# Optimization experiments

Hardware: AMD Instinct MI355X
Metric: run time of the kernel (lower is better)

## Reference

```python
import jax, jax.numpy as jnp
import numpy as np

N, K, C, L = 8192, 12, 128, 6
FF = 4 * C
SIG_LO, SIG_HI = 1.0, 5.0
BOX = 25.0

TRI_NAMES = ("ln_g", "ln_b", "Wa", "ba", "Wga", "bga", "Wb", "bb", "Wgb", "bgb",
             "lno_g", "lno_b", "Wo", "bo", "Wgo", "bgo")
FFN_NAMES = ("ln_g", "ln_b", "W1", "b1", "W2", "b2")


def _ln(x, g, b, eps=1e-5):
    m = jnp.mean(x, axis=-1, keepdims=True)
    v = jnp.mean((x - m) ** 2, axis=-1, keepdims=True)
    return (x - m) * jax.lax.rsqrt(v + eps) * g + b


def _knn_embed(coords):
    # pairwise distances -> k smallest (self included), Gaussian RBF bank over C sigmas
    d2 = jnp.sum((coords[:, None, :] - coords[None, :, :]) ** 2, axis=-1)  # [N,N]
    dist = jnp.sqrt(jnp.maximum(d2, 0.0))
    neg_d, nbr = jax.lax.top_k(-dist, K)                      # [N,K]
    k_dist = -neg_d
    sig = jnp.linspace(SIG_LO, SIG_HI, C)                     # [C]
    g = jnp.exp(-(k_dist[..., None] ** 2) / (2.0 * sig ** 2))  # [N,K,C]
    vals = jnp.where(g > 0.1, g, 0.0)                         # threshold as in repo
    vals = jnp.where(jnp.isnan(vals), 0.0, vals)
    return nbr, vals


def _transpose_vals(v, nbr):
    # sparse rowcol_transpose: value of edge (j,i) aligned to slot of edge (i,j); 0 if absent
    n = nbr.shape[0]
    nn = nbr[nbr]                                   # [N,K,K]: neighbor lists of each neighbor j
    eq = nn == jnp.arange(n)[:, None, None]         # slot where j lists i back
    pos = jnp.argmax(eq, axis=-1)                   # [N,K]
    found = jnp.any(eq, axis=-1)                    # [N,K]
    tv = v[nbr, pos]                                # [N,K,C] value at edge (j,i)
    return jnp.where(found[..., None], tv, jnp.zeros_like(tv))


def _tri_update(v, nbr, p, incoming):
    x = _ln(v, p["ln_g"], p["ln_b"])
    a = jax.nn.sigmoid(x @ p["Wga"] + p["bga"]) * (x @ p["Wa"] + p["ba"])
    b = jax.nn.sigmoid(x @ p["Wgb"] + p["bgb"]) * (x @ p["Wb"] + p["bb"])
    if incoming:  # column/incoming update operates on transposed edges
        a = _transpose_vals(a, nbr)
        b = _transpose_vals(b, nbr)
    # sparse triangle multiplicative update over KNN neighbor slots
    k = jnp.einsum('ntc,nmtc->nmc', a, b[nbr])      # [N,K,C]
    o = _ln(k, p["lno_g"], p["lno_b"]) @ p["Wo"] + p["bo"]
    return jax.nn.sigmoid(x @ p["Wgo"] + p["bgo"]) * o


def _ffn(v, p):
    x = _ln(v, p["ln_g"], p["ln_b"])
    return jax.nn.gelu(x @ p["W1"] + p["b1"], approximate=False) @ p["W2"] + p["b2"]


def _forward(coords, tri, ffn, dec_W, dec_b):
    nbr, v = _knn_embed(coords)
    v = jax.lax.stop_gradient(v)  # embedding runs under torch.no_grad in the original

    def step(v, lp):
        tp, fp = lp
        p_row = {n: t[0] for n, t in zip(TRI_NAMES, tp)}
        p_col = {n: t[1] for n, t in zip(TRI_NAMES, tp)}
        v = v + _tri_update(v, nbr, p_row, False)   # row (outgoing) update
        v = v + _tri_update(v, nbr, p_col, True)    # col (incoming) update
        v = v + _ffn(v, dict(zip(FFN_NAMES, fp)))
        return v, None

    v, _ = jax.lax.scan(jax.checkpoint(step), v, (tri, ffn))
    s = v + _transpose_vals(v, nbr)                 # sparse_operation(edge, edge^T, op='sum')
    e = s @ dec_W + dec_b                           # [N,K,1] decode
    rows = jnp.repeat(jnp.arange(N), K)
    dense = jnp.zeros((N, N, e.shape[-1]), e.dtype)
    dense = dense.at[rows, nbr.reshape(-1)].add(e.reshape(-1, e.shape[-1]))
    return dense                                    # [N,N,1] like .to_dense()


def setup_inputs() -> dict:
    key = jax.random.key(0)
    ks = jax.random.split(key, 8)
    coords = jax.random.uniform(ks[0], (N, 3), jnp.float32) * BOX

    def lin(k, fin, fout, pre=()):
        kw, _ = jax.random.split(k)
        W = jax.random.normal(kw, pre + (fin, fout), jnp.float32) / np.sqrt(fin).astype(np.float32)
        b = jnp.zeros(pre + (fout,), jnp.float32)
        return W, b

    inp = {"coords": coords}
    k_iter = iter(jax.random.split(ks[1], 16))
    pre = (L, 2)
    inp["tri_ln_g"] = jnp.ones(pre + (C,), jnp.float32)
    inp["tri_ln_b"] = jnp.zeros(pre + (C,), jnp.float32)
    for nm in ("a", "ga", "b", "gb", "o", "go"):
        W, b = lin(next(k_iter), C, C, pre)
        inp[f"tri_W{nm}"] = W
        inp[f"tri_b{nm}"] = b
    inp["tri_lno_g"] = jnp.ones(pre + (C,), jnp.float32)
    inp["tri_lno_b"] = jnp.zeros(pre + (C,), jnp.float32)
    inp["ffn_ln_g"] = jnp.ones((L, C), jnp.float32)
    inp["ffn_ln_b"] = jnp.zeros((L, C), jnp.float32)
    inp["ffn_W1"], inp["ffn_b1"] = lin(next(k_iter), C, FF, (L,))
    inp["ffn_W2"], inp["ffn_b2"] = lin(next(k_iter), FF, C, (L,))
    inp["dec_W"], inp["dec_b"] = lin(next(k_iter), C, 1)
    return inp


def reference(coords, tri_ln_g, tri_ln_b, tri_Wa, tri_ba, tri_Wga, tri_bga,
              tri_Wb, tri_bb, tri_Wgb, tri_bgb, tri_lno_g, tri_lno_b,
              tri_Wo, tri_bo, tri_Wgo, tri_bgo,
              ffn_ln_g, ffn_ln_b, ffn_W1, ffn_b1, ffn_W2, ffn_b2,
              dec_W, dec_b):
    tri = (tri_ln_g, tri_ln_b, tri_Wa, tri_ba, tri_Wga, tri_bga,
           tri_Wb, tri_bb, tri_Wgb, tri_bgb, tri_lno_g, tri_lno_b,
           tri_Wo, tri_bo, tri_Wgo, tri_bgo)
    ffn = (ffn_ln_g, ffn_ln_b, ffn_W1, ffn_b1, ffn_W2, ffn_b2)
    return _forward(coords, tri, ffn, dec_W, dec_b)
```

## Files before the change

kernel.cpp:

```cpp
#include <hip/hip_runtime.h>
#include <hip/hip_bf16.h>
#include <stdint.h>
#include <stddef.h>

#define NPTS 8192
#define KNN  12
#define CH   128
#define FFD  512
#define MEDGE (NPTS * KNN)
#define NCELL 512

typedef __attribute__((ext_vector_type(8))) _Float16 half8;
typedef __attribute__((ext_vector_type(4))) _Float16 half4;
typedef __attribute__((ext_vector_type(4))) float f32x4;

__device__ __forceinline__ float wave_sum(float v) {
#pragma unroll
  for (int off = 32; off > 0; off >>= 1) v += __shfl_xor(v, off, 64);
  return v;
}
__device__ __forceinline__ float sigm_(float x) { return 1.0f / (1.0f + expf(-x)); }
__device__ __forceinline__ float gelu_(float x) { return 0.5f * x * (1.0f + erff(x * 0.7071067811865475f)); }

#define HADDR(row, ch) ((((row) * 64 + ((ch) ^ ((row) & 7)))) * 8)

__device__ __forceinline__ int morton3(int x, int y, int z) {
  int m = 0;
#pragma unroll
  for (int b = 0; b < 3; ++b)
    m |= (((x >> b) & 1) << (3 * b + 2)) | (((y >> b) & 1) << (3 * b + 1)) | (((z >> b) & 1) << (3 * b));
  return m;
}

__global__ __launch_bounds__(512)
void zero_hist(int* __restrict__ hist)
{
  hist[threadIdx.x] = 0;
}

__global__ __launch_bounds__(256)
void prep_coords(const float* __restrict__ c, float4* __restrict__ c4,
                 int* __restrict__ cell, int* __restrict__ hist)
{
  int i = blockIdx.x * 256 + threadIdx.x;
  if (i >= NPTS) return;
  float x = c[3 * i], y = c[3 * i + 1], z = c[3 * i + 2];
  c4[i] = make_float4(x, y, z, 0.0f);
  int cx = (int)(x * (8.0f / 25.0f)); if (cx > 7) cx = 7; if (cx < 0) cx = 0;
  int cy = (int)(y * (8.0f / 25.0f)); if (cy > 7) cy = 7; if (cy < 0) cy = 0;
  int cz = (int)(z * (8.0f / 25.0f)); if (cz > 7) cz = 7; if (cz < 0) cz = 0;
  int cl = morton3(cx, cy, cz);
  cell[i] = cl;
  atomicAdd(&hist[cl], 1);
}

__global__ __launch_bounds__(512)
void prefix512(const int* __restrict__ hist, int* __restrict__ base)
{
  __shared__ int tmp[NCELL];
  int t = threadIdx.x;
  tmp[t] = hist[t];
  __syncthreads();
  for (int off = 1; off < NCELL; off <<= 1) {
    int v = tmp[t];
    if (t >= off) v += tmp[t - off];
    __syncthreads();
    tmp[t] = v;
    __syncthreads();
  }
  base[t] = tmp[t] - hist[t];
}

__global__ __launch_bounds__(256)
void scatter_perm(const int* __restrict__ cell, int* __restrict__ base,
                  int* __restrict__ rank, int* __restrict__ perm)
{
  int i = blockIdx.x * 256 + threadIdx.x;
  if (i >= NPTS) return;
  int r = atomicAdd(&base[cell[i]], 1);
  rank[i] = r;
  perm[r] = i;
}

struct SwzArgs {
  const float* src[8];
  _Float16* dst[8];
  int K[8], N[8], B[8], perB[8];
};

__global__ __launch_bounds__(256)
void prep_weights_swz(SwzArgs sa)
{
  int g = blockIdx.y;
  int idx = blockIdx.x * 256 + threadIdx.x;
  int perB = sa.perB[g];
  if (idx >= sa.B[g] * perB) return;
  int K = sa.K[g], N = sa.N[g];
  int b = idx / perB;
  int c = idx - b * perB;
  int l16 = c & 15;
  int quad = (c >> 4) & 3;
  int rest = c >> 6;
  int kts = K >> 5;
  int kt = rest % kts;
  int mt = rest / kts;
  const float* sp = sa.src[g] + ((size_t)b * K + kt * 32 + quad * 8) * N + mt * 16 + l16;
  _Float16* dp = sa.dst[g] + ((size_t)b * perB + c) * 8;
#pragma unroll
  for (int e = 0; e < 8; ++e) dp[e] = (_Float16)sp[(size_t)e * N];
}

#define KNN_CAP 2048

__global__ __launch_bounds__(256)
void knn_embed(const float4* __restrict__ coords4, const int* __restrict__ perm,
               const int* __restrict__ rank,
               const float* __restrict__ lng, const float* __restrict__ lnb,
               int* __restrict__ nbr, float* __restrict__ v0, _Float16* __restrict__ xln)
{
#pragma clang fp contract(off)
  __shared__ unsigned long long buf[KNN_CAP];
  __shared__ unsigned long long sel[KNN];
  __shared__ int cnt_s;
  const int i = blockIdx.x;
  const int tid = threadIdx.x;
  const int lane = tid & 63;
  const int wv = tid >> 6;
  const float4 ci = coords4[perm[i]];

  float T2 = 9.0f;
  int cnt;
  while (true) {
    if (tid == 0) cnt_s = 0;
    __syncthreads();
    for (int j = tid; j < NPTS; j += 256) {
      float4 cj = coords4[j];
      float dx = ci.x - cj.x;
      float dy = ci.y - cj.y;
      float dz = ci.z - cj.z;
      float d2 = dx * dx + dy * dy + dz * dz;
      if (d2 < T2) {
        unsigned long long key =
            (((unsigned long long)__float_as_uint(sqrtf(d2))) << 32) | (unsigned int)j;
        int idx = atomicAdd(&cnt_s, 1);
        if (idx < KNN_CAP) buf[idx] = key;
      }
    }
    __syncthreads();
    cnt = cnt_s;
    if (cnt >= KNN) break;
    T2 *= 4.0f;
    __syncthreads();
  }
  if (cnt > KNN_CAP) cnt = KNN_CAP;

  if (wv == 0) {
    unsigned long long best[KNN];
#pragma unroll
    for (int q = 0; q < KNN; ++q) best[q] = ~0ULL;
    for (int p2 = lane; p2 < cnt; p2 += 64) {
      unsigned long long key = buf[p2];
      if (key < best[KNN - 1]) {
        best[KNN - 1] = key;
#pragma unroll
        for (int q = KNN - 2; q >= 0; --q) {
          if (best[q + 1] < best[q]) { unsigned long long t = best[q]; best[q] = best[q + 1]; best[q + 1] = t; }
        }
      }
    }
    int p = 0;
    for (int r = 0; r < KNN; ++r) {
      unsigned long long c = ~0ULL;
#pragma unroll
      for (int q = 0; q < KNN; ++q) if (q == p) c = best[q];
      unsigned long long m = c;
#pragma unroll
      for (int off = 32; off > 0; off >>= 1) {
        unsigned long long o = __shfl_xor(m, off, 64);
        if (o < m) m = o;
      }
      if (c == m) ++p;
      if (lane == 0) sel[r] = m;
    }
  }
  __syncthreads();
  if (tid < KNN)
    nbr[i * KNN + tid] = rank[(int)(unsigned int)(sel[tid] & 0xFFFFFFFFULL)];

  float g1 = lng[lane], g2 = lng[lane + 64];
  float bb1 = lnb[lane], bb2 = lnb[lane + 64];
  for (int k = wv * 3; k < wv * 3 + 3; ++k) {
    float d = __uint_as_float((unsigned int)(sel[k] >> 32));
    float sig1 = (float)(1.0 + 4.0 * (double)lane / 127.0);
    float sig2 = (float)(1.0 + 4.0 * (double)(lane + 64) / 127.0);
    float e1 = expf((-(d * d)) / (2.0f * sig1 * sig1));
    float e2 = expf((-(d * d)) / (2.0f * sig2 * sig2));
    float v1 = (e1 > 0.1f) ? e1 : 0.0f;
    float v2 = (e2 > 0.1f) ? e2 : 0.0f;
    size_t off = (size_t)(i * KNN + k) * CH;
    v0[off + lane] = v1;
    v0[off + lane + 64] = v2;
    float m = wave_sum(v1 + v2) * (1.0f / 128.0f);
    float d1 = v1 - m, d2 = v2 - m;
    float var = wave_sum(d1 * d1 + d2 * d2) * (1.0f / 128.0f);
    float rs = 1.0f / sqrtf(var + 1e-5f);
    xln[off + lane]      = (_Float16)(d1 * rs * g1 + bb1);
    xln[off + lane + 64] = (_Float16)(d2 * rs * g2 + bb2);
  }
}

__global__ __launch_bounds__(256)
void build_tidx(const int* __restrict__ nbr, int* __restrict__ tidx)
{
  int e = blockIdx.x * 256 + threadIdx.x;
  if (e >= MEDGE) return;
  int i = e / KNN;
  int j = nbr[e];
  int res = -1;
#pragma unroll
  for (int t = 0; t < KNN; ++t) {
    if (nbr[j * KNN + t] == i) { res = j * KNN + t; break; }
  }
  tidx[e] = res;
}

__global__ __launch_bounds__(256)
void gemm_ab_go(const _Float16* __restrict__ xln,
                const _Float16* __restrict__ wa,  const float* __restrict__ ba,
                const _Float16* __restrict__ wga, const float* __restrict__ bga,
                const _Float16* __restrict__ wb,  const float* __restrict__ bb,
                const _Float16* __restrict__ wgb, const float* __restrict__ bgb,
                const _Float16* __restrict__ wgo, const float* __restrict__ bgo,
                _Float16* __restrict__ aout, _Float16* __restrict__ bout,
                _Float16* __restrict__ gobout)
{
  const int lane = threadIdx.x & 63;
  const int quad = lane >> 4;
  const int l16 = lane & 15;
  const int gw = blockIdx.x * 4 + (threadIdx.x >> 6);
  const int base = gw * 32;
  const int chbase = quad * 16 + l16;

  half8 xf[2][4];
#pragma unroll
  for (int rt = 0; rt < 2; ++rt)
#pragma unroll
    for (int kt = 0; kt < 4; ++kt)
      xf[rt][kt] = *(const half8*)(xln + (size_t)(base + rt * 16 + l16) * CH + kt * 32 + quad * 8);

  const half8* WA  = (const half8*)wa;
  const half8* WGA = (const half8*)wga;
  const half8* WB  = (const half8*)wb;
  const half8* WGB = (const half8*)wgb;
  const half8* WGO = (const half8*)wgo;

#pragma unroll
  for (int mt = 0; mt < 8; ++mt) {
    f32x4 aA[2], aGA[2], aB[2], aGB[2], aGO[2];
    const f32x4 z = {0.f, 0.f, 0.f, 0.f};
#pragma unroll
    for (int rt = 0; rt < 2; ++rt) { aA[rt] = z; aGA[rt] = z; aB[rt] = z; aGB[rt] = z; aGO[rt] = z; }
#pragma unroll
    for (int kt = 0; kt < 4; ++kt) {
      int ch = (mt * 4 + kt) * 64 + chbase;
      half8 wfa = WA[ch], wfga = WGA[ch], wfb = WB[ch], wfgb = WGB[ch], wfgo = WGO[ch];
#pragma unroll
      for (int rt = 0; rt < 2; ++rt) {
        aA[rt]  = __builtin_amdgcn_mfma_f32_16x16x32_f16(wfa,  xf[rt][kt], aA[rt], 0, 0, 0);
        aGA[rt] = __builtin_amdgcn_mfma_f32_16x16x32_f16(wfga, xf[rt][kt], aGA[rt], 0, 0, 0);
        aB[rt]  = __builtin_amdgcn_mfma_f32_16x16x32_f16(wfb,  xf[rt][kt], aB[rt], 0, 0, 0);
        aGB[rt] = __builtin_amdgcn_mfma_f32_16x16x32_f16(wfgb, xf[rt][kt], aGB[rt], 0, 0, 0);
        aGO[rt] = __builtin_amdgcn_mfma_f32_16x16x32_f16(wfgo, xf[rt][kt], aGO[rt], 0, 0, 0);
      }
    }
    f32x4 bva  = *(const f32x4*)(ba  + mt * 16 + quad * 4);
    f32x4 bvga = *(const f32x4*)(bga + mt * 16 + quad * 4);
    f32x4 bvb  = *(const f32x4*)(bb  + mt * 16 + quad * 4);
    f32x4 bvgb = *(const f32x4*)(bgb + mt * 16 + quad * 4);
    f32x4 bvgo = *(const f32x4*)(bgo + mt * 16 + quad * 4);
#pragma unroll
    for (int rt = 0; rt < 2; ++rt) {
      half4 av, bv, gv;
#pragma unroll
      for (int r = 0; r < 4; ++r) {
        av[r] = (_Float16)(sigm_(aGA[rt][r] + bvga[r]) * (aA[rt][r] + bva[r]));
        bv[r] = (_Float16)(sigm_(aGB[rt][r] + bvgb[r]) * (aB[rt][r] + bvb[r]));
        gv[r] = (_Float16)(sigm_(aGO[rt][r] + bvgo[r]));
      }
      size_t off = (size_t)(base + rt * 16 + l16) * CH + mt * 16 + quad * 4;
      *(half4*)(aout + off) = av;
      *(half4*)(bout + off) = bv;
      *(half4*)(gobout + off) = gv;
    }
  }
}

__global__ __launch_bounds__(192)
void tri_og(const _Float16* __restrict__ a, const _Float16* __restrict__ b,
            const int* __restrict__ nbr, const int* __restrict__ tidx,
            const float* __restrict__ lng, const float* __restrict__ lnb,
            const _Float16* __restrict__ wo, const float* __restrict__ bo,
            const _Float16* __restrict__ gob, float* __restrict__ v,
            const float* __restrict__ nlng, const float* __restrict__ nlnb,
            _Float16* __restrict__ xlnN, int incoming)
{
  __shared__ alignas(16) _Float16 As[48][136];
  __shared__ alignas(16) _Float16 klds[48][136];
  __shared__ int bidx[4][KNN][KNN];
  __shared__ int nbr_s[4][KNN];
  const int blk = blockIdx.x;
  const int n0 = ((blk & 7) * 256 + (blk >> 3)) * 4;
  const int tid = threadIdx.x;

  if (tid < 48) nbr_s[tid / KNN][tid % KNN] = nbr[n0 * KNN + tid];
  __syncthreads();
  for (int it = tid; it < 4 * KNN * KNN; it += 192) {
    int nn = it / (KNN * KNN);
    int r = it - nn * KNN * KNN;
    int m = r / KNN, t = r - m * KNN;
    int j = nbr_s[nn][m];
    bidx[nn][m][t] = incoming ? tidx[j * KNN + t] : (j * KNN + t);
  }
  for (int it = tid; it < 4 * KNN * 16; it += 192) {
    int nn = it / (KNN * 16);
    int r = it - nn * (KNN * 16);
    int t = r >> 4;
    int c8 = (r & 15) * 8;
    half8 av;
    if (incoming) {
      int ti = tidx[(size_t)(n0 + nn) * KNN + t];
      if (ti >= 0) av = *(const half8*)(a + (size_t)ti * CH + c8);
      else {
#pragma unroll
        for (int e = 0; e < 8; ++e) av[e] = (_Float16)0.0f;
      }
    } else {
      av = *(const half8*)(a + (size_t)((n0 + nn) * KNN + t) * CH + c8);
    }
    *(half8*)&As[nn * KNN + t][c8] = av;
  }
  __syncthreads();

  const int m2 = tid >> 4;
  const int c8 = (tid & 15) * 8;
  for (int nn = 0; nn < 4; ++nn) {
    float acc[8];
#pragma unroll
    for (int r = 0; r < 8; ++r) acc[r] = 0.0f;
#pragma unroll
    for (int t = 0; t < KNN; ++t) {
      int bi = bidx[nn][m2][t];
      if (bi >= 0) {
        half8 bv = *(const half8*)(b + (size_t)bi * CH + c8);
        half8 av = *(const half8*)&As[nn * KNN + t][c8];
#pragma unroll
        for (int r = 0; r < 8; ++r) acc[r] += (float)av[r] * (float)bv[r];
      }
    }
    float s = 0.0f, sq = 0.0f;
#pragma unroll
    for (int r = 0; r < 8; ++r) { s += acc[r]; sq += acc[r] * acc[r]; }
#pragma unroll
    for (int off = 1; off < 16; off <<= 1) {
      s += __shfl_xor(s, off, 64);
      sq += __shfl_xor(sq, off, 64);
    }
    float mean = s * (1.0f / 128.0f);
    float var = sq * (1.0f / 128.0f) - mean * mean;
    if (var < 0.0f) var = 0.0f;
    float rs = 1.0f / sqrtf(var + 1e-5f);
    half8 o;
#pragma unroll
    for (int r = 0; r < 8; ++r)
      o[r] = (_Float16)((acc[r] - mean) * rs * lng[c8 + r] + lnb[c8 + r]);
    *(half8*)&klds[nn * KNN + m2][c8] = o;
  }
  __syncthreads();

  const int lane = tid & 63;
  const int w = tid >> 6;
  const int quad = lane >> 4;
  const int l16 = lane & 15;
  const int chbase = quad * 16 + l16;
  const size_t rowOff = (size_t)(n0 * KNN + w * 16 + l16) * CH;

  half8 kf[4];
#pragma unroll
  for (int kt = 0; kt < 4; ++kt)
    kf[kt] = *(const half8*)&klds[w * 16 + l16][kt * 32 + quad * 8];

  const half8* WO = (const half8*)wo;
  f32x4 vn[8];
  float s = 0.0f, sq = 0.0f;
#pragma unroll
  for (int mt = 0; mt < 8; ++mt) {
    f32x4 acc = {0.f, 0.f, 0.f, 0.f};
#pragma unroll
    for (int kt = 0; kt < 4; ++kt)
      acc = __builtin_amdgcn_mfma_f32_16x16x32_f16(WO[(mt * 4 + kt) * 64 + chbase], kf[kt], acc, 0, 0, 0);
    half4 g4 = *(const half4*)(gob + rowOff + mt * 16 + quad * 4);
    f32x4 bo4 = *(const f32x4*)(bo + mt * 16 + quad * 4);
    f32x4 vv = *(const f32x4*)(v + rowOff + mt * 16 + quad * 4);
#pragma unroll
    for (int r = 0; r < 4; ++r) {
      float nv = vv[r] + (float)g4[r] * (acc[r] + bo4[r]);
      vn[mt][r] = nv;
      s += nv;
      sq += nv * nv;
    }
    *(f32x4*)(v + rowOff + mt * 16 + quad * 4) = vn[mt];
  }
  s  += __shfl_xor(s, 16, 64);  s  += __shfl_xor(s, 32, 64);
  sq += __shfl_xor(sq, 16, 64); sq += __shfl_xor(sq, 32, 64);
  float mean = s * (1.0f / 128.0f);
  float var = sq * (1.0f / 128.0f) - mean * mean;
  if (var < 0.0f) var = 0.0f;
  float rs = 1.0f / sqrtf(var + 1e-5f);
#pragma unroll
  for (int mt = 0; mt < 8; ++mt) {
    f32x4 g4 = *(const f32x4*)(nlng + mt * 16 + quad * 4);
    f32x4 b4 = *(const f32x4*)(nlnb + mt * 16 + quad * 4);
    half4 o;
#pragma unroll
    for (int r = 0; r < 4; ++r)
      o[r] = (_Float16)((vn[mt][r] - mean) * rs * g4[r] + b4[r]);
    *(half4*)(xlnN + rowOff + mt * 16 + quad * 4) = o;
  }
}

__global__ __launch_bounds__(256)
void ffn_fused(const _Float16* __restrict__ xln,
               const _Float16* __restrict__ w1, const float* __restrict__ b1,
               const _Float16* __restrict__ w2, const float* __restrict__ b2,
               float* __restrict__ v,
               const float* __restrict__ nlng, const float* __restrict__ nlnb,
               _Float16* __restrict__ xlnN)
{
  __shared__ alignas(16) _Float16 hlds[32 * FFD];
  __shared__ float part[32][4][2];
  const int tid = threadIdx.x;
  const int lane = tid & 63;
  const int w = tid >> 6;
  const int quad = lane >> 4;
  const int l16 = lane & 15;
  const int rowBase = blockIdx.x * 32;
  const int chbase = quad * 16 + l16;

  half8 xf[2][4];
#pragma unroll
  for (int rt = 0; rt < 2; ++rt)
#pragma unroll
    for (int kt = 0; kt < 4; ++kt)
      xf[rt][kt] = *(const half8*)(xln + (size_t)(rowBase + rt * 16 + l16) * CH + kt * 32 + quad * 8);

  const half8* W1 = (const half8*)w1;
#pragma unroll
  for (int mt = 0; mt < 8; ++mt) {
    int mtg = w * 8 + mt;
    f32x4 acc[2];
    const f32x4 z = {0.f, 0.f, 0.f, 0.f};
    acc[0] = z; acc[1] = z;
#pragma unroll
    for (int kt = 0; kt < 4; ++kt) {
      half8 wf = W1[(mtg * 4 + kt) * 64 + chbase];
#pragma unroll
      for (int rt = 0; rt < 2; ++rt)
        acc[rt] = __builtin_amdgcn_mfma_f32_16x16x32_f16(wf, xf[rt][kt], acc[rt], 0, 0, 0);
    }
    f32x4 bv = *(const f32x4*)(b1 + mtg * 16 + quad * 4);
    int ch = mtg * 2 + (quad >> 1);
    int sub = (quad & 1) * 4;
#pragma unroll
    for (int rt = 0; rt < 2; ++rt) {
      int row = rt * 16 + l16;
      half4 hh;
#pragma unroll
      for (int r = 0; r < 4; ++r)
        hh[r] = (_Float16)(gelu_(acc[rt][r] + bv[r]));
      *(half4*)&hlds[HADDR(row, ch) + sub] = hh;
    }
  }
  __syncthreads();

  const half8* W2 = (const half8*)w2;
  f32x4 vn2[2][2];
  float s2[2] = {0.f, 0.f}, q2[2] = {0.f, 0.f};
#pragma unroll
  for (int m2 = 0; m2 < 2; ++m2) {
    int mt = w * 2 + m2;
    f32x4 accA[2], accB[2];
    const f32x4 z = {0.f, 0.f, 0.f, 0.f};
    accA[0] = z; accA[1] = z; accB[0] = z; accB[1] = z;
#pragma unroll
    for (int kt = 0; kt < 16; kt += 2) {
      half8 wf0 = W2[(mt * 16 + kt) * 64 + chbase];
      half8 wf1 = W2[(mt * 16 + kt + 1) * 64 + chbase];
#pragma unroll
      for (int rt = 0; rt < 2; ++rt) {
        int row = rt * 16 + l16;
        half8 hf0 = *(const half8*)&hlds[HADDR(row, kt * 4 + quad)];
        half8 hf1 = *(const half8*)&hlds[HADDR(row, (kt + 1) * 4 + quad)];
        accA[rt] = __builtin_amdgcn_mfma_f32_16x16x32_f16(wf0, hf0, accA[rt], 0, 0, 0);
        accB[rt] = __builtin_amdgcn_mfma_f32_16x16x32_f16(wf1, hf1, accB[rt], 0, 0, 0);
      }
    }
    f32x4 bv = *(const f32x4*)(b2 + mt * 16 + quad * 4);
#pragma unroll
    for (int rt = 0; rt < 2; ++rt) {
      size_t off = (size_t)(rowBase + rt * 16 + l16) * CH + mt * 16 + quad * 4;
      f32x4 vv = *(const f32x4*)(v + off);
#pragma unroll
      for (int r = 0; r < 4; ++r) {
        float nv = vv[r] + accA[rt][r] + accB[rt][r] + bv[r];
        vn2[m2][rt][r] = nv;
        s2[rt] += nv;
        q2[rt] += nv * nv;
      }
      *(f32x4*)(v + off) = vn2[m2][rt];
    }
  }
#pragma unroll
  for (int rt = 0; rt < 2; ++rt) {
    float ss = s2[rt], qq = q2[rt];
    ss += __shfl_xor(ss, 16, 64); ss += __shfl_xor(ss, 32, 64);
    qq += __shfl_xor(qq, 16, 64); qq += __shfl_xor(qq, 32, 64);
    if (quad == 0) { part[rt * 16 + l16][w][0] = ss; part[rt * 16 + l16][w][1] = qq; }
  }
  __syncthreads();
#pragma unroll
  for (int rt = 0; rt < 2; ++rt) {
    int row = rt * 16 + l16;
    float su = part[row][0][0] + part[row][1][0] + part[row][2][0] + part[row][3][0];
    float qu = part[row][0][1] + part[row][1][1] + part[row][2][1] + part[row][3][1];
    float mean = su * (1.0f / 128.0f);
    float var = qu * (1.0f / 128.0f) - mean * mean;
    if (var < 0.0f) var = 0.0f;
    float rs = 1.0f / sqrtf(var + 1e-5f);
#pragma unroll
    for (int m2 = 0; m2 < 2; ++m2) {
      int mt = w * 2 + m2;
      f32x4 g4 = *(const f32x4*)(nlng + mt * 16 + quad * 4);
      f32x4 b4 = *(const f32x4*)(nlnb + mt * 16 + quad * 4);
      half4 o;
#pragma unroll
      for (int r = 0; r < 4; ++r)
        o[r] = (_Float16)((vn2[m2][rt][r] - mean) * rs * g4[r] + b4[r]);
      *(half4*)(xlnN + (size_t)(rowBase + row) * CH + mt * 16 + quad * 4) = o;
    }
  }
}

__global__ __launch_bounds__(256)
void decode_row(const float* __restrict__ vin, const int* __restrict__ tidx,
                const int* __restrict__ nbr, const int* __restrict__ perm,
                const float* __restrict__ decW, const float* __restrict__ decB,
                float* __restrict__ out)
{
  __shared__ float ev[KNN];
  __shared__ int col_s[KNN];
  const int n = blockIdx.x;
  const int tid = threadIdx.x;
  const int lane = tid & 63;
  const int w = tid >> 6;
  if (tid < KNN) col_s[tid] = perm[nbr[n * KNN + tid]];
  float dw1 = decW[lane], dw2 = decW[lane + 64];
  for (int k = w; k < KNN; k += 4) {
    int e = n * KNN + k;
    int ti = tidx[e];
    float s1 = vin[(size_t)e * CH + lane];
    float s2 = vin[(size_t)e * CH + 64 + lane];
    if (ti >= 0) {
      s1 += vin[(size_t)ti * CH + lane];
      s2 += vin[(size_t)ti * CH + 64 + lane];
    }
    float tot = wave_sum(s1 * dw1 + s2 * dw2);
    if (lane == 0) ev[k] = tot + decB[0];
  }
  __syncthreads();
  const int orig_n = perm[n];
  float4 z = make_float4(0.f, 0.f, 0.f, 0.f);
  float4* row = (float4*)(out + (size_t)orig_n * NPTS);
  for (int idx = tid; idx < NPTS / 4; idx += 256) row[idx] = z;
  __syncthreads();
  if (tid < KNN) out[(size_t)orig_n * NPTS + col_s[tid]] = ev[tid];
}

extern "C" void kernel_launch(void* const* d_in, const int* in_sizes, int n_in,
                              void* d_out, int out_size, void* d_ws, size_t ws_size,
                              hipStream_t stream)
{
  (void)in_sizes; (void)n_in; (void)out_size; (void)ws_size;
  const float* coords  = (const float*)d_in[0];
  const float* t_ln_g  = (const float*)d_in[1];
  const float* t_ln_b  = (const float*)d_in[2];
  const float* t_Wa    = (const float*)d_in[3];
  const float* t_ba    = (const float*)d_in[4];
  const float* t_Wga   = (const float*)d_in[5];
  const float* t_bga   = (const float*)d_in[6];
  const float* t_Wb    = (const float*)d_in[7];
  const float* t_bb    = (const float*)d_in[8];
  const float* t_Wgb   = (const float*)d_in[9];
  const float* t_bgb   = (const float*)d_in[10];
  const float* t_Wo    = (const float*)d_in[11];
  const float* t_bo    = (const float*)d_in[12];
  const float* t_Wgo   = (const float*)d_in[13];
  const float* t_bgo   = (const float*)d_in[14];
  const float* t_lno_g = (const float*)d_in[15];
  const float* t_lno_b = (const float*)d_in[16];
  const float* f_ln_g  = (const float*)d_in[17];
  const float* f_ln_b  = (const float*)d_in[18];
  const float* f_W1    = (const float*)d_in[19];
  const float* f_b1    = (const float*)d_in[20];
  const float* f_W2    = (const float*)d_in[21];
  const float* f_b2    = (const float*)d_in[22];
  const float* dec_W   = (const float*)d_in[23];
  const float* dec_b   = (const float*)d_in[24];

  const size_t NKC = (size_t)MEDGE * CH;
  char* ws = (char*)d_ws;
  float* v        = (float*)(ws);
  _Float16* gx    = (_Float16*)(ws + NKC * 6);
  int* nbr        = (int*)(ws + NKC * 8);
  int* tidx       = (int*)(ws + NKC * 8 + (size_t)MEDGE * 4);
  char* aux       = ws + NKC * 8 + (size_t)MEDGE * 8;
  float4* coords4 = (float4*)(aux);
  int* cell       = (int*)(aux + NPTS * 16);
  int* hist       = (int*)(aux + NPTS * 16 + NPTS * 4);
  int* base       = (int*)(aux + NPTS * 16 + NPTS * 4 + NCELL * 4);
  int* rank       = (int*)(aux + NPTS * 16 + NPTS * 4 + NCELL * 8);
  int* perm       = (int*)(aux + NPTS * 16 + NPTS * 8 + NCELL * 8);
  _Float16* wbase = (_Float16*)(aux + NPTS * 16 + NPTS * 12 + NCELL * 8);
  const size_t TRIH = (size_t)12 * 2048 * 8;
  _Float16* wA  = wbase;
  _Float16* wGA = wA  + TRIH;
  _Float16* wB  = wGA + TRIH;
  _Float16* wGB = wB  + TRIH;
  _Float16* wGO = wGB + TRIH;
  _Float16* wO  = wGO + TRIH;
  _Float16* w1  = wO  + TRIH;
  _Float16* w2  = w1  + (size_t)6 * 8192 * 8;

  _Float16* abuf = (_Float16*)d_out;
  _Float16* bbuf = abuf + NKC;

  zero_hist<<<1, 512, 0, stream>>>(hist);
  prep_coords<<<32, 256, 0, stream>>>(coords, coords4, cell, hist);
  prefix512<<<1, 512, 0, stream>>>(hist, base);
  scatter_perm<<<32, 256, 0, stream>>>(cell, base, rank, perm);

  SwzArgs sa;
  sa.src[0] = t_Wa;  sa.dst[0] = wA;  sa.K[0] = CH;  sa.N[0] = CH;  sa.B[0] = 12; sa.perB[0] = 2048;
  sa.src[1] = t_Wga; sa.dst[1] = wGA; sa.K[1] = CH;  sa.N[1] = CH;  sa.B[1] = 12; sa.perB[1] = 2048;
  sa.src[2] = t_Wb;  sa.dst[2] = wB;  sa.K[2] = CH;  sa.N[2] = CH;  sa.B[2] = 12; sa.perB[2] = 2048;
  sa.src[3] = t_Wgb; sa.dst[3] = wGB; sa.K[3] = CH;  sa.N[3] = CH;  sa.B[3] = 12; sa.perB[3] = 2048;
  sa.src[4] = t_Wgo; sa.dst[4] = wGO; sa.K[4] = CH;  sa.N[4] = CH;  sa.B[4] = 12; sa.perB[4] = 2048;
  sa.src[5] = t_Wo;  sa.dst[5] = wO;  sa.K[5] = CH;  sa.N[5] = CH;  sa.B[5] = 12; sa.perB[5] = 2048;
  sa.src[6] = f_W1;  sa.dst[6] = w1;  sa.K[6] = CH;  sa.N[6] = FFD; sa.B[6] = 6;  sa.perB[6] = 8192;
  sa.src[7] = f_W2;  sa.dst[7] = w2;  sa.K[7] = FFD; sa.N[7] = CH;  sa.B[7] = 6;  sa.perB[7] = 8192;
  dim3 pgrid(192, 8);
  prep_weights_swz<<<pgrid, 256, 0, stream>>>(sa);

  knn_embed<<<NPTS, 256, 0, stream>>>(coords4, perm, rank, t_ln_g, t_ln_b, nbr, v, gx);
  build_tidx<<<MEDGE / 256, 256, 0, stream>>>(nbr, tidx);

  const size_t WS = (size_t)2048 * 8;
  gemm_ab_go<<<MEDGE / 128, 256, 0, stream>>>(gx,
      wA, t_ba, wGA, t_bga, wB, t_bb, wGB, t_bgb, wGO, t_bgo,
      abuf, bbuf, gx);

  for (int l = 0; l < 6; ++l) {
    int s0 = 2 * l, s1 = 2 * l + 1, s2 = 2 * l + 2;
    tri_og<<<NPTS / 4, 192, 0, stream>>>(abuf, bbuf, nbr, tidx,
        t_lno_g + s0 * CH, t_lno_b + s0 * CH,
        wO + s0 * WS, t_bo + s0 * CH, gx, v,
        t_ln_g + s1 * CH, t_ln_b + s1 * CH, gx, 0);
    gemm_ab_go<<<MEDGE / 128, 256, 0, stream>>>(gx,
        wA + s1 * WS, t_ba + s1 * CH, wGA + s1 * WS, t_bga + s1 * CH,
        wB + s1 * WS, t_bb + s1 * CH, wGB + s1 * WS, t_bgb + s1 * CH,
        wGO + s1 * WS, t_bgo + s1 * CH,
        abuf, bbuf, gx);
    tri_og<<<NPTS / 4, 192, 0, stream>>>(abuf, bbuf, nbr, tidx,
        t_lno_g + s1 * CH, t_lno_b + s1 * CH,
        wO + s1 * WS, t_bo + s1 * CH, gx, v,
        f_ln_g + l * CH, f_ln_b + l * CH, gx, 1);
    const float* ng = (l < 5) ? (t_ln_g + s2 * CH) : t_ln_g;
    const float* nb = (l < 5) ? (t_ln_b + s2 * CH) : t_ln_b;
    ffn_fused<<<MEDGE / 32, 256, 0, stream>>>(gx,
        w1 + (size_t)l * 8192 * 8, f_b1 + l * FFD,
        w2 + (size_t)l * 8192 * 8, f_b2 + l * CH,
        v, ng, nb, gx);
    if (l < 5) {
      gemm_ab_go<<<MEDGE / 128, 256, 0, stream>>>(gx,
          wA + s2 * WS, t_ba + s2 * CH, wGA + s2 * WS, t_bga + s2 * CH,
          wB + s2 * WS, t_bb + s2 * CH, wGB + s2 * WS, t_bgb + s2 * CH,
          wGO + s2 * WS, t_bgo + s2 * CH,
          abuf, bbuf, gx);
    }
  }

  decode_row<<<NPTS, 256, 0, stream>>>(v, tidx, nbr, perm, dec_W, dec_b, (float*)d_out);
}
```

Baseline: 2.435 ms.

## Fuse next-layer gated A/B projections into FFN kernel and drop A staging in tri_og

```diff
diff --git a/kernel.cpp b/kernel.cpp
--- a/kernel.cpp
+++ b/kernel.cpp
@@ -23,6 +23,7 @@
 __device__ __forceinline__ float gelu_(float x) { return 0.5f * x * (1.0f + erff(x * 0.7071067811865475f)); }
 
 #define HADDR(row, ch) ((((row) * 64 + ((ch) ^ ((row) & 7)))) * 8)
+#define XADDR(row, ch) ((((row) * 16 + ((ch) ^ ((row) & 7)))) * 8)
 
 __device__ __forceinline__ int morton3(int x, int y, int z) {
   int m = 0;
@@ -304,9 +305,9 @@
             const float* __restrict__ nlng, const float* __restrict__ nlnb,
             _Float16* __restrict__ xlnN, int incoming)
 {
-  __shared__ alignas(16) _Float16 As[48][136];
   __shared__ alignas(16) _Float16 klds[48][136];
   __shared__ int bidx[4][KNN][KNN];
+  __shared__ int aidx[4][KNN];
   __shared__ int nbr_s[4][KNN];
   const int blk = blockIdx.x;
   const int n0 = ((blk & 7) * 256 + (blk >> 3)) * 4;
@@ -321,23 +322,9 @@
     int j = nbr_s[nn][m];
     bidx[nn][m][t] = incoming ? tidx[j * KNN + t] : (j * KNN + t);
   }
-  for (int it = tid; it < 4 * KNN * 16; it += 192) {
-    int nn = it / (KNN * 16);
-    int r = it - nn * (KNN * 16);
-    int t = r >> 4;
-    int c8 = (r & 15) * 8;
-    half8 av;
-    if (incoming) {
-      int ti = tidx[(size_t)(n0 + nn) * KNN + t];
-      if (ti >= 0) av = *(const half8*)(a + (size_t)ti * CH + c8);
-      else {
-#pragma unroll
-        for (int e = 0; e < 8; ++e) av[e] = (_Float16)0.0f;
-      }
-    } else {
-      av = *(const half8*)(a + (size_t)((n0 + nn) * KNN + t) * CH + c8);
-    }
-    *(half8*)&As[nn * KNN + t][c8] = av;
+  if (tid < 48) {
+    int nn = tid / KNN, t = tid % KNN;
+    aidx[nn][t] = incoming ? tidx[(size_t)(n0 + nn) * KNN + t] : ((n0 + nn) * KNN + t);
   }
   __syncthreads();
 
@@ -349,10 +336,11 @@
     for (int r = 0; r < 8; ++r) acc[r] = 0.0f;
 #pragma unroll
     for (int t = 0; t < KNN; ++t) {
+      int ai = aidx[nn][t];
       int bi = bidx[nn][m2][t];
-      if (bi >= 0) {
+      if (ai >= 0 && bi >= 0) {
         half8 bv = *(const half8*)(b + (size_t)bi * CH + c8);
-        half8 av = *(const half8*)&As[nn * KNN + t][c8];
+        half8 av = *(const half8*)(a + (size_t)ai * CH + c8);
 #pragma unroll
         for (int r = 0; r < 8; ++r) acc[r] += (float)av[r] * (float)bv[r];
       }
@@ -429,12 +417,18 @@
 }
 
 __global__ __launch_bounds__(256)
-void ffn_fused(const _Float16* __restrict__ xln,
-               const _Float16* __restrict__ w1, const float* __restrict__ b1,
-               const _Float16* __restrict__ w2, const float* __restrict__ b2,
-               float* __restrict__ v,
-               const float* __restrict__ nlng, const float* __restrict__ nlnb,
-               _Float16* __restrict__ xlnN)
+void ffn_ab(const _Float16* __restrict__ xln,
+            const _Float16* __restrict__ w1, const float* __restrict__ b1,
+            const _Float16* __restrict__ w2, const float* __restrict__ b2,
+            float* __restrict__ v,
+            const float* __restrict__ nlng, const float* __restrict__ nlnb,
+            const _Float16* __restrict__ wa,  const float* __restrict__ ba,
+            const _Float16* __restrict__ wga, const float* __restrict__ bga,
+            const _Float16* __restrict__ wb,  const float* __restrict__ bb,
+            const _Float16* __restrict__ wgb, const float* __restrict__ bgb,
+            const _Float16* __restrict__ wgo2, const float* __restrict__ bgo2,
+            _Float16* __restrict__ aout, _Float16* __restrict__ bout,
+            _Float16* __restrict__ gobout, int doAB)
 {
   __shared__ alignas(16) _Float16 hlds[32 * FFD];
   __shared__ float part[32][4][2];
@@ -519,6 +513,8 @@
       *(f32x4*)(v + off) = vn2[m2][rt];
     }
   }
+  if (!doAB) return;
+
 #pragma unroll
   for (int rt = 0; rt < 2; ++rt) {
     float ss = s2[rt], qq = q2[rt];
@@ -527,6 +523,8 @@
     if (quad == 0) { part[rt * 16 + l16][w][0] = ss; part[rt * 16 + l16][w][1] = qq; }
   }
   __syncthreads();
+
+  _Float16* xsw = hlds;
 #pragma unroll
   for (int rt = 0; rt < 2; ++rt) {
     int row = rt * 16 + l16;
@@ -545,7 +543,62 @@
 #pragma unroll
       for (int r = 0; r < 4; ++r)
         o[r] = (_Float16)((vn2[m2][rt][r] - mean) * rs * g4[r] + b4[r]);
-      *(half4*)(xlnN + (size_t)(rowBase + row) * CH + mt * 16 + quad * 4) = o;
+      int ch = mt * 2 + (quad >> 1);
+      *(half4*)&xsw[XADDR(row, ch) + (quad & 1) * 4] = o;
+    }
+  }
+  __syncthreads();
+
+  half8 xfD[2][4];
+#pragma unroll
+  for (int rt = 0; rt < 2; ++rt)
+#pragma unroll
+    for (int kt = 0; kt < 4; ++kt)
+      xfD[rt][kt] = *(const half8*)&xsw[XADDR(rt * 16 + l16, kt * 4 + quad)];
+
+  const half8* WA  = (const half8*)wa;
+  const half8* WGA = (const half8*)wga;
+  const half8* WB  = (const half8*)wb;
+  const half8* WGB = (const half8*)wgb;
+  const half8* WGO = (const half8*)wgo2;
+#pragma unroll
+  for (int m2 = 0; m2 < 2; ++m2) {
+    int mt = w * 2 + m2;
+    f32x4 aA[2], aGA[2], aB[2], aGB[2], aGO[2];
+    const f32x4 z = {0.f, 0.f, 0.f, 0.f};
+#pragma unroll
+    for (int rt = 0; rt < 2; ++rt) { aA[rt] = z; aGA[rt] = z; aB[rt] = z; aGB[rt] = z; aGO[rt] = z; }
+#pragma unroll
+    for (int kt = 0; kt < 4; ++kt) {
+      int ch = (mt * 4 + kt) * 64 + chbase;
+      half8 wfa = WA[ch], wfga = WGA[ch], wfb = WB[ch], wfgb = WGB[ch], wfgo = WGO[ch];
+#pragma unroll
+      for (int rt = 0; rt < 2; ++rt) {
+        aA[rt]  = __builtin_amdgcn_mfma_f32_16x16x32_f16(wfa,  xfD[rt][kt], aA[rt], 0, 0, 0);
+        aGA[rt] = __builtin_amdgcn_mfma_f32_16x16x32_f16(wfga, xfD[rt][kt], aGA[rt], 0, 0, 0);
+        aB[rt]  = __builtin_amdgcn_mfma_f32_16x16x32_f16(wfb,  xfD[rt][kt], aB[rt], 0, 0, 0);
+        aGB[rt] = __builtin_amdgcn_mfma_f32_16x16x32_f16(wfgb, xfD[rt][kt], aGB[rt], 0, 0, 0);
+        aGO[rt] = __builtin_amdgcn_mfma_f32_16x16x32_f16(wfgo, xfD[rt][kt], aGO[rt], 0, 0, 0);
+      }
+    }
+    f32x4 bva  = *(const f32x4*)(ba   + mt * 16 + quad * 4);
+    f32x4 bvga = *(const f32x4*)(bga  + mt * 16 + quad * 4);
+    f32x4 bvb  = *(const f32x4*)(bb   + mt * 16 + quad * 4);
+    f32x4 bvgb = *(const f32x4*)(bgb  + mt * 16 + quad * 4);
+    f32x4 bvgo = *(const f32x4*)(bgo2 + mt * 16 + quad * 4);
+#pragma unroll
+    for (int rt = 0; rt < 2; ++rt) {
+      half4 av, bv, gv;
+#pragma unroll
+      for (int r = 0; r < 4; ++r) {
+        av[r] = (_Float16)(sigm_(aGA[rt][r] + bvga[r]) * (aA[rt][r] + bva[r]));
+        bv[r] = (_Float16)(sigm_(aGB[rt][r] + bvgb[r]) * (aB[rt][r] + bvb[r]));
+        gv[r] = (_Float16)(sigm_(aGO[rt][r] + bvgo[r]));
+      }
+      size_t off = (size_t)(rowBase + rt * 16 + l16) * CH + mt * 16 + quad * 4;
+      *(half4*)(aout + off) = av;
+      *(half4*)(bout + off) = bv;
+      *(half4*)(gobout + off) = gv;
     }
   }
 }
@@ -683,19 +736,16 @@
         t_lno_g + s1 * CH, t_lno_b + s1 * CH,
         wO + s1 * WS, t_bo + s1 * CH, gx, v,
         f_ln_g + l * CH, f_ln_b + l * CH, gx, 1);
-    const float* ng = (l < 5) ? (t_ln_g + s2 * CH) : t_ln_g;
-    const float* nb = (l < 5) ? (t_ln_b + s2 * CH) : t_ln_b;
-    ffn_fused<<<MEDGE / 32, 256, 0, stream>>>(gx,
+    int doAB = (l < 5) ? 1 : 0;
+    int sw = doAB ? s2 : 0;
+    ffn_ab<<<MEDGE / 32, 256, 0, stream>>>(gx,
         w1 + (size_t)l * 8192 * 8, f_b1 + l * FFD,
         w2 + (size_t)l * 8192 * 8, f_b2 + l * CH,
-        v, ng, nb, gx);
-    if (l < 5) {
-      gemm_ab_go<<<MEDGE / 128, 256, 0, stream>>>(gx,
-          wA + s2 * WS, t_ba + s2 * CH, wGA + s2 * WS, t_bga + s2 * CH,
-          wB + s2 * WS, t_bb + s2 * CH, wGB + s2 * WS, t_bgb + s2 * CH,
-          wGO + s2 * WS, t_bgo + s2 * CH,
-          abuf, bbuf, gx);
-    }
+        v, t_ln_g + sw * CH, t_ln_b + sw * CH,
+        wA + sw * WS, t_ba + sw * CH, wGA + sw * WS, t_bga + sw * CH,
+        wB + sw * WS, t_bb + sw * CH, wGB + sw * WS, t_bgb + sw * CH,
+        wGO + sw * WS, t_bgo + sw * CH,
+        abuf, bbuf, gx, doAB);
   }
 
   decode_row<<<NPTS, 256, 0, stream>>>(v, tidx, nbr, perm, dec_W, dec_b, (float*)d_out);
```

Measured after the change: 2.956 ms. 21.4% more time.
